# Performance work log

Hardware: AMD Instinct MI355X
Metric: run time of the kernel (lower is better)

Reference implementation:

```python
import jax, jax.numpy as jnp
import numpy as np

B, T, C, H = 4, 2048, 1024, 128

def setup_inputs() -> dict:
    key = jax.random.key(0)
    k1, k2, k3, k4 = jax.random.split(key, 4)
    x = jax.random.normal(k1, (B, T, C), dtype=jnp.float32)
    # nn.Linear(C, H, bias=False) weights, stored as [C, H] so y = x @ W
    scale = 1.0 / np.sqrt(C)
    Wq = jax.random.normal(k2, (C, H), dtype=jnp.float32) * scale
    Wk = jax.random.normal(k3, (C, H), dtype=jnp.float32) * scale
    Wv = jax.random.normal(k4, (C, H), dtype=jnp.float32) * scale
    mask = jnp.tril(jnp.ones((T, T), dtype=jnp.int32))  # causal mask
    return {"x": x, "Wq": Wq, "Wk": Wk, "Wv": Wv, "mask": mask}

def reference(x, Wq, Wk, Wv, mask):
    # x: [B,T,C]; projections to [B,T,H]
    q = jnp.einsum("btc,ch->bth", x, Wq)
    k = jnp.einsum("btc,ch->bth", x, Wk)
    v = jnp.einsum("btc,ch->bth", x, Wv)
    # NOTE: original scales by C**-0.5 (embedding dim), not head_size**-0.5
    inv_scale = x.shape[-1] ** (-0.5)
    scores = jnp.einsum("bth,bsh->bts", q, k) * inv_scale  # [B,T,T]
    scores = jnp.where(mask == 0, -jnp.inf, scores)
    weights = jax.nn.softmax(scores, axis=-1)
    # Dropout(0.1) is identity in eval mode
    return jnp.einsum("bts,bsh->bth", weights, v)  # [B,T,H]
```

## Files before the change

### kernel.cpp

```cpp
#include <hip/hip_runtime.h>
#include <hip/hip_bf16.h>
#include <cstdint>


typedef __bf16 bf16_t;
typedef __bf16 bf16x4 __attribute__((ext_vector_type(4)));
typedef __bf16 bf16x8 __attribute__((ext_vector_type(8)));
typedef float f32x4 __attribute__((ext_vector_type(4)));

#define MFMA16(a, b, c) __builtin_amdgcn_mfma_f32_16x16x32_bf16(a, b, c, 0, 0, 0)

constexpr int T = 2048;
constexpr int C = 1024;
constexpr int H = 128;

__device__ inline bf16x8 load8f(const float* __restrict__ p) {
    float4 a = *(const float4*)p;
    float4 b = *(const float4*)(p + 4);
    bf16x8 r;
    r[0] = (bf16_t)a.x; r[1] = (bf16_t)a.y; r[2] = (bf16_t)a.z; r[3] = (bf16_t)a.w;
    r[4] = (bf16_t)b.x; r[5] = (bf16_t)b.y; r[6] = (bf16_t)b.z; r[7] = (bf16_t)b.w;
    return r;
}

__global__ __launch_bounds__(256) void convert_x(const float* __restrict__ x,
                                                 bf16_t* __restrict__ xb, int n8) {
    int i = blockIdx.x * 256 + threadIdx.x;
    const int stride = gridDim.x * 256;
    for (; i < n8; i += stride)
        *(bf16x8*)(xb + (size_t)i * 8) = load8f(x + (size_t)i * 8);
}

__global__ void transpose_w(const float* __restrict__ Wq,
                            const float* __restrict__ Wk,
                            const float* __restrict__ Wv,
                            bf16_t* __restrict__ Wt) {
    __shared__ bf16_t tile[32][34];
    const float* W = blockIdx.z == 0 ? Wq : (blockIdx.z == 1 ? Wk : Wv);
    const int c0 = blockIdx.x * 32, h0 = blockIdx.y * 32;
    const int tx = threadIdx.x, ty = threadIdx.y;
#pragma unroll
    for (int i = 0; i < 4; i++)
        tile[ty + 8 * i][tx] = (bf16_t)W[(size_t)(c0 + ty + 8 * i) * H + h0 + tx];
    __syncthreads();
    bf16_t* Wtz = Wt + (size_t)blockIdx.z * H * C;
#pragma unroll
    for (int i = 0; i < 4; i++)
        Wtz[(size_t)(h0 + ty + 8 * i) * C + c0 + tx] = tile[tx][ty + 8 * i];
}

__global__ __launch_bounds__(256) void proj_gemm(const bf16_t* __restrict__ xb,
                                                 const bf16_t* __restrict__ Wt,
                                                 bf16_t* __restrict__ qout,
                                                 bf16_t* __restrict__ kout,
                                                 bf16_t* __restrict__ vtout) {
    const int w = threadIdx.x >> 6;
    const int wm = w & 1, wn = w >> 1;
    const int lane = threadIdx.x & 63;
    const int m16 = lane & 15, g = lane >> 4;
    const int z = blockIdx.y;
    const int m0 = blockIdx.x * 64 + wm * 32;
    const int n0 = wn * 64;

    const bf16_t* arow = xb + (size_t)(m0 + m16) * C + g * 8;
    const bf16_t* brow = Wt + (size_t)(z * H + n0 + m16) * C + g * 8;

    f32x4 zero = {0.f, 0.f, 0.f, 0.f};
    f32x4 acc[2][4];
#pragma unroll
    for (int mf = 0; mf < 2; mf++)
#pragma unroll
        for (int nf = 0; nf < 4; nf++) acc[mf][nf] = zero;

    bf16x8 a0 = *(const bf16x8*)(arow);
    bf16x8 a1 = *(const bf16x8*)(arow + 16 * C);
    bf16x8 bb[4];
#pragma unroll
    for (int nf = 0; nf < 4; nf++) bb[nf] = *(const bf16x8*)(brow + (size_t)nf * 16 * C);

    for (int k0 = 0; k0 < C - 32; k0 += 32) {
        bf16x8 na0 = *(const bf16x8*)(arow + k0 + 32);
        bf16x8 na1 = *(const bf16x8*)(arow + 16 * C + k0 + 32);
        bf16x8 nb[4];
#pragma unroll
        for (int nf = 0; nf < 4; nf++)
            nb[nf] = *(const bf16x8*)(brow + (size_t)nf * 16 * C + k0 + 32);
#pragma unroll
        for (int nf = 0; nf < 4; nf++) {
            acc[0][nf] = MFMA16(a0, bb[nf], acc[0][nf]);
            acc[1][nf] = MFMA16(a1, bb[nf], acc[1][nf]);
        }
        a0 = na0; a1 = na1;
#pragma unroll
        for (int nf = 0; nf < 4; nf++) bb[nf] = nb[nf];
    }
#pragma unroll
    for (int nf = 0; nf < 4; nf++) {
        acc[0][nf] = MFMA16(a0, bb[nf], acc[0][nf]);
        acc[1][nf] = MFMA16(a1, bb[nf], acc[1][nf]);
    }

    if (z < 2) {
        bf16_t* out = (z == 0) ? qout : kout;
#pragma unroll
        for (int mf = 0; mf < 2; mf++)
#pragma unroll
            for (int nf = 0; nf < 4; nf++)
#pragma unroll
                for (int ri = 0; ri < 4; ri++) {
                    int r = m0 + mf * 16 + g * 4 + ri;
                    out[(size_t)r * H + n0 + nf * 16 + m16] = (bf16_t)acc[mf][nf][ri];
                }
    } else {
#pragma unroll
        for (int mf = 0; mf < 2; mf++) {
            const int t0 = m0 + mf * 16 + g * 4;
            const int bidx = t0 >> 11, t = t0 & (T - 1);
#pragma unroll
            for (int nf = 0; nf < 4; nf++) {
                const int h = n0 + nf * 16 + m16;
                bf16x4 v;
#pragma unroll
                for (int ri = 0; ri < 4; ri++) v[ri] = (bf16_t)acc[mf][nf][ri];
                *(bf16x4*)(vtout + ((size_t)bidx * H + h) * T + t) = v;
            }
        }
    }
}

__global__ __launch_bounds__(256) void attn(const bf16_t* __restrict__ q,
                                            const bf16_t* __restrict__ k,
                                            const bf16_t* __restrict__ vt,
                                            float* __restrict__ out) {
    __shared__ float accw[4][16][128];
    __shared__ __align__(16) bf16_t pbuf[4][16][40];
    __shared__ float mred[4][16], lred[4][16];
    const int w = threadIdx.x >> 6;
    const int lane = threadIdx.x & 63;
    const int m16 = lane & 15, g = lane >> 4;
    const int b = blockIdx.x & 3;
    const int kk = blockIdx.x >> 2;
    const int qt = (kk < 64) ? kk : 191 - kk;
    const int q0 = qt * 16;

    const bf16_t* qb = q + (size_t)b * T * H;
    const bf16_t* kb = k + (size_t)b * T * H;
    const bf16_t* vb = vt + (size_t)b * H * T;

    bf16x8 aq[4];
#pragma unroll
    for (int c = 0; c < 4; c++)
        aq[c] = *(const bf16x8*)(qb + (size_t)(q0 + m16) * H + c * 32 + g * 8);

    bf16x8 ones;
#pragma unroll
    for (int j = 0; j < 8; j++) ones[j] = (bf16_t)1.0f;

    f32x4 zero = {0.f, 0.f, 0.f, 0.f};
    f32x4 acc[9];
#pragma unroll
    for (int ht = 0; ht < 9; ht++) acc[ht] = zero;
    float mst[4];
#pragma unroll
    for (int ri = 0; ri < 4; ri++) mst[ri] = -1e30f;

    const int kv_end = q0 + 16;
    for (int kv0 = w * 32; kv0 < kv_end; kv0 += 128) {
        f32x4 s[2];
        s[0] = zero; s[1] = zero;
#pragma unroll
        for (int t = 0; t < 2; t++)
#pragma unroll
            for (int c = 0; c < 4; c++) {
                bf16x8 bk = *(const bf16x8*)(kb + (size_t)(kv0 + t * 16 + m16) * H + c * 32 + g * 8);
                s[t] = MFMA16(aq[c], bk, s[t]);
            }

        float p0v[4], p1v[4];
#pragma unroll
        for (int ri = 0; ri < 4; ri++) {
            const int row = q0 + g * 4 + ri;
            float v0 = s[0][ri] * 0.03125f;
            float v1 = s[1][ri] * 0.03125f;
            if (kv0 + m16 > row) v0 = -1e30f;
            if (kv0 + 16 + m16 > row) v1 = -1e30f;
            float rm = fmaxf(v0, v1);
#pragma unroll
            for (int off = 1; off < 16; off <<= 1) rm = fmaxf(rm, __shfl_xor(rm, off));
            const float mnew = fmaxf(mst[ri], rm);
            const float alpha = __expf(mst[ri] - mnew);
            mst[ri] = mnew;
            p0v[ri] = __expf(v0 - mnew);
            p1v[ri] = __expf(v1 - mnew);
#pragma unroll
            for (int ht = 0; ht < 9; ht++) acc[ht][ri] *= alpha;
        }

#pragma unroll
        for (int ri = 0; ri < 4; ri++) {
            pbuf[w][g * 4 + ri][m16] = (bf16_t)p0v[ri];
            pbuf[w][g * 4 + ri][16 + m16] = (bf16_t)p1v[ri];
        }
        bf16x8 ap = *(const bf16x8*)(&pbuf[w][m16][g * 8]);

#pragma unroll
        for (int ht = 0; ht < 8; ht++) {
            bf16x8 bv = *(const bf16x8*)(vb + (size_t)(ht * 16 + m16) * T + kv0 + g * 8);
            acc[ht] = MFMA16(ap, bv, acc[ht]);
        }
        acc[8] = MFMA16(ap, ones, acc[8]);
    }

    if (m16 == 0) {
#pragma unroll
        for (int ri = 0; ri < 4; ri++) mred[w][g * 4 + ri] = mst[ri];
    }
    __syncthreads();
    float scale[4];
#pragma unroll
    for (int ri = 0; ri < 4; ri++) {
        const int row = g * 4 + ri;
        float mt = fmaxf(fmaxf(mred[0][row], mred[1][row]),
                         fmaxf(mred[2][row], mred[3][row]));
        scale[ri] = __expf(mst[ri] - mt);
    }
    if (m16 == 0) {
#pragma unroll
        for (int ri = 0; ri < 4; ri++) lred[w][g * 4 + ri] = acc[8][ri] * scale[ri];
    }
#pragma unroll
    for (int ht = 0; ht < 8; ht++)
#pragma unroll
        for (int ri = 0; ri < 4; ri++)
            accw[w][g * 4 + ri][ht * 16 + m16] = acc[ht][ri] * scale[ri];
    __syncthreads();

    float* ob = out + ((size_t)b * T + q0) * H;
    for (int e = threadIdx.x; e < 16 * 128; e += 256) {
        const int row = e >> 7, col = e & 127;
        float o = accw[0][row][col] + accw[1][row][col] +
                  accw[2][row][col] + accw[3][row][col];
        float l = lred[0][row] + lred[1][row] + lred[2][row] + lred[3][row];
        ob[(size_t)row * H + col] = o / l;
    }
}

extern "C" void kernel_launch(void* const* d_in, const int* in_sizes, int n_in,
                              void* d_out, int out_size, void* d_ws, size_t ws_size,
                              hipStream_t stream) {
    const float* x = (const float*)d_in[0];
    const float* Wq = (const float*)d_in[1];
    const float* Wk = (const float*)d_in[2];
    const float* Wv = (const float*)d_in[3];
    float* out = (float*)d_out;

    char* ws = (char*)d_ws;
    bf16_t* xb = (bf16_t*)ws;
    bf16_t* Wt = (bf16_t*)(ws + 16777216);
    char* p = ws + 16777216 + 786432;
    bf16_t* qb = (bf16_t*)(p);
    bf16_t* kb = (bf16_t*)(p + 2097152);
    bf16_t* vt = (bf16_t*)(p + 2 * 2097152);

    hipLaunchKernelGGL(convert_x, dim3(2048), dim3(256), 0, stream,
                       x, xb, (int)((size_t)4 * T * C / 8));
    hipLaunchKernelGGL(transpose_w, dim3(C / 32, H / 32, 3), dim3(32, 8), 0, stream,
                       Wq, Wk, Wv, Wt);
    hipLaunchKernelGGL(proj_gemm, dim3(128, 3), dim3(256), 0, stream,
                       xb, Wt, qb, kb, vt);
    hipLaunchKernelGGL(attn, dim3(512), dim3(256), 0, stream,
                       qb, kb, vt, out);
}
```

Before: 170.0 us.

## Split projection GEMM tiles, deepen its prefetch, and prefetch K/V in attention

The projection GEMM now tiles N into two 64-wide halves per block (grid 128x2x3), which doubles the block count, and uses a 4-deep register prefetch ring over K. The C^-0.5 scale is folded into Q at projection time, removing the per-score multiply in attention. The attention kernel now prefetches the next K tile and issues V loads ahead of the softmax, so global latency overlaps with compute. The cost is higher register pressure, plus an extra rounding step because Q is scaled before the bf16 cast.

New measurement: 170.6 us. Within noise of the previous version (+0.3%).

```diff
diff --git a/kernel.cpp b/kernel.cpp
--- a/kernel.cpp
+++ b/kernel.cpp
@@ -58,54 +58,52 @@
     const int wm = w & 1, wn = w >> 1;
     const int lane = threadIdx.x & 63;
     const int m16 = lane & 15, g = lane >> 4;
-    const int z = blockIdx.y;
+    const int z = blockIdx.z;
     const int m0 = blockIdx.x * 64 + wm * 32;
-    const int n0 = wn * 64;
-
-    const bf16_t* arow = xb + (size_t)(m0 + m16) * C + g * 8;
-    const bf16_t* brow = Wt + (size_t)(z * H + n0 + m16) * C + g * 8;
+    const int n0 = blockIdx.y * 64 + wn * 32;
+
+    const bf16_t* a0p = xb + (size_t)(m0 + m16) * C + g * 8;
+    const bf16_t* a1p = a0p + (size_t)16 * C;
+    const bf16_t* b0p = Wt + (size_t)(z * H + n0 + m16) * C + g * 8;
+    const bf16_t* b1p = b0p + (size_t)16 * C;
 
     f32x4 zero = {0.f, 0.f, 0.f, 0.f};
-    f32x4 acc[2][4];
-#pragma unroll
-    for (int mf = 0; mf < 2; mf++)
-#pragma unroll
-        for (int nf = 0; nf < 4; nf++) acc[mf][nf] = zero;
-
-    bf16x8 a0 = *(const bf16x8*)(arow);
-    bf16x8 a1 = *(const bf16x8*)(arow + 16 * C);
-    bf16x8 bb[4];
-#pragma unroll
-    for (int nf = 0; nf < 4; nf++) bb[nf] = *(const bf16x8*)(brow + (size_t)nf * 16 * C);
-
-    for (int k0 = 0; k0 < C - 32; k0 += 32) {
-        bf16x8 na0 = *(const bf16x8*)(arow + k0 + 32);
-        bf16x8 na1 = *(const bf16x8*)(arow + 16 * C + k0 + 32);
-        bf16x8 nb[4];
-#pragma unroll
-        for (int nf = 0; nf < 4; nf++)
-            nb[nf] = *(const bf16x8*)(brow + (size_t)nf * 16 * C + k0 + 32);
-#pragma unroll
-        for (int nf = 0; nf < 4; nf++) {
-            acc[0][nf] = MFMA16(a0, bb[nf], acc[0][nf]);
-            acc[1][nf] = MFMA16(a1, bb[nf], acc[1][nf]);
-        }
-        a0 = na0; a1 = na1;
-#pragma unroll
-        for (int nf = 0; nf < 4; nf++) bb[nf] = nb[nf];
-    }
-#pragma unroll
-    for (int nf = 0; nf < 4; nf++) {
-        acc[0][nf] = MFMA16(a0, bb[nf], acc[0][nf]);
-        acc[1][nf] = MFMA16(a1, bb[nf], acc[1][nf]);
-    }
+    f32x4 acc00 = zero, acc01 = zero, acc10 = zero, acc11 = zero;
+
+    bf16x8 pa0[4], pa1[4], pb0[4], pb1[4];
+#pragma unroll
+    for (int j = 0; j < 4; j++) {
+        pa0[j] = *(const bf16x8*)(a0p + j * 32);
+        pa1[j] = *(const bf16x8*)(a1p + j * 32);
+        pb0[j] = *(const bf16x8*)(b0p + j * 32);
+        pb1[j] = *(const bf16x8*)(b1p + j * 32);
+    }
+
+#pragma unroll
+    for (int j = 0; j < C / 32; j++) {
+        const int s = j & 3;
+        acc00 = MFMA16(pa0[s], pb0[s], acc00);
+        acc01 = MFMA16(pa0[s], pb1[s], acc01);
+        acc10 = MFMA16(pa1[s], pb0[s], acc10);
+        acc11 = MFMA16(pa1[s], pb1[s], acc11);
+        const int kn = (j + 4) * 32;
+        if (kn < C) {
+            pa0[s] = *(const bf16x8*)(a0p + kn);
+            pa1[s] = *(const bf16x8*)(a1p + kn);
+            pb0[s] = *(const bf16x8*)(b0p + kn);
+            pb1[s] = *(const bf16x8*)(b1p + kn);
+        }
+    }
+
+    const float sc = (z == 0) ? 0.03125f : 1.0f;
+    f32x4 acc[2][2] = {{acc00 * sc, acc01 * sc}, {acc10 * sc, acc11 * sc}};
 
     if (z < 2) {
         bf16_t* out = (z == 0) ? qout : kout;
 #pragma unroll
         for (int mf = 0; mf < 2; mf++)
 #pragma unroll
-            for (int nf = 0; nf < 4; nf++)
+            for (int nf = 0; nf < 2; nf++)
 #pragma unroll
                 for (int ri = 0; ri < 4; ri++) {
                     int r = m0 + mf * 16 + g * 4 + ri;
@@ -117,7 +115,7 @@
             const int t0 = m0 + mf * 16 + g * 4;
             const int bidx = t0 >> 11, t = t0 & (T - 1);
 #pragma unroll
-            for (int nf = 0; nf < 4; nf++) {
+            for (int nf = 0; nf < 2; nf++) {
                 const int h = n0 + nf * 16 + m16;
                 bf16x4 v;
 #pragma unroll
@@ -165,23 +163,44 @@
     for (int ri = 0; ri < 4; ri++) mst[ri] = -1e30f;
 
     const int kv_end = q0 + 16;
-    for (int kv0 = w * 32; kv0 < kv_end; kv0 += 128) {
+    bf16x8 kc[8], kn[8], vc[8];
+    int kv0 = w * 32;
+    if (kv0 < kv_end) {
+#pragma unroll
+        for (int t = 0; t < 2; t++)
+#pragma unroll
+            for (int c = 0; c < 4; c++)
+                kc[t * 4 + c] = *(const bf16x8*)(kb + (size_t)(kv0 + t * 16 + m16) * H + c * 32 + g * 8);
+    }
+
+    for (; kv0 < kv_end; kv0 += 128) {
         f32x4 s[2];
         s[0] = zero; s[1] = zero;
 #pragma unroll
         for (int t = 0; t < 2; t++)
 #pragma unroll
-            for (int c = 0; c < 4; c++) {
-                bf16x8 bk = *(const bf16x8*)(kb + (size_t)(kv0 + t * 16 + m16) * H + c * 32 + g * 8);
-                s[t] = MFMA16(aq[c], bk, s[t]);
-            }
+            for (int c = 0; c < 4; c++)
+                s[t] = MFMA16(aq[c], kc[t * 4 + c], s[t]);
+
+#pragma unroll
+        for (int ht = 0; ht < 8; ht++)
+            vc[ht] = *(const bf16x8*)(vb + (size_t)(ht * 16 + m16) * T + kv0 + g * 8);
+
+        const int kvn = kv0 + 128;
+        if (kvn < kv_end) {
+#pragma unroll
+            for (int t = 0; t < 2; t++)
+#pragma unroll
+                for (int c = 0; c < 4; c++)
+                    kn[t * 4 + c] = *(const bf16x8*)(kb + (size_t)(kvn + t * 16 + m16) * H + c * 32 + g * 8);
+        }
 
         float p0v[4], p1v[4];
 #pragma unroll
         for (int ri = 0; ri < 4; ri++) {
             const int row = q0 + g * 4 + ri;
-            float v0 = s[0][ri] * 0.03125f;
-            float v1 = s[1][ri] * 0.03125f;
+            float v0 = s[0][ri];
+            float v1 = s[1][ri];
             if (kv0 + m16 > row) v0 = -1e30f;
             if (kv0 + 16 + m16 > row) v1 = -1e30f;
             float rm = fmaxf(v0, v1);
@@ -204,11 +223,12 @@
         bf16x8 ap = *(const bf16x8*)(&pbuf[w][m16][g * 8]);
 
 #pragma unroll
-        for (int ht = 0; ht < 8; ht++) {
-            bf16x8 bv = *(const bf16x8*)(vb + (size_t)(ht * 16 + m16) * T + kv0 + g * 8);
-            acc[ht] = MFMA16(ap, bv, acc[ht]);
-        }
+        for (int ht = 0; ht < 8; ht++)
+            acc[ht] = MFMA16(ap, vc[ht], acc[ht]);
         acc[8] = MFMA16(ap, ones, acc[8]);
+
+#pragma unroll
+        for (int i = 0; i < 8; i++) kc[i] = kn[i];
     }
 
     if (m16 == 0) {
@@ -266,7 +286,7 @@
                        x, xb, (int)((size_t)4 * T * C / 8));
     hipLaunchKernelGGL(transpose_w, dim3(C / 32, H / 32, 3), dim3(32, 8), 0, stream,
                        Wq, Wk, Wv, Wt);
-    hipLaunchKernelGGL(proj_gemm, dim3(128, 3), dim3(256), 0, stream,
+    hipLaunchKernelGGL(proj_gemm, dim3(128, 2, 3), dim3(256), 0, stream,
                        xb, Wt, qb, kb, vt);
     hipLaunchKernelGGL(attn, dim3(512), dim3(256), 0, stream,
                        qb, kb, vt, out);
```
